# Performance work log

Hardware: AMD Instinct MI355X
Metric: run time of the kernel (lower is better)

The kernel has to match this reference:

```python
import jax, jax.numpy as jnp
from jax import lax
import numpy as np

B, DIM, HEADS, H, W = 4, 384, 8, 128, 128


def conv2d(x, w, b, groups=1, pad=0):
    # x: NCHW, w: OIHW (I = in_channels // groups)
    y = lax.conv_general_dilated(
        x, w, window_strides=(1, 1), padding=[(pad, pad), (pad, pad)],
        dimension_numbers=("NCHW", "OIHW", "NCHW"), feature_group_count=groups)
    return y + b[None, :, None, None]


def _l2norm(x, eps=1e-12):
    # torch F.normalize(dim=-1): x / max(||x||_2, eps)
    n = jnp.sqrt(jnp.sum(x * x, axis=-1, keepdims=True))
    return x / jnp.maximum(n, eps)


def setup_inputs() -> dict:
    key = jax.random.key(0)
    ks = jax.random.split(key, 8)
    s = 0.02
    d = DIM
    return {
        "x": jax.random.normal(ks[0], (B, d, H, W), jnp.float32),
        "feature": jax.random.normal(ks[1], (B, d, H, W), jnp.float32),
        "qkv_w": jax.random.normal(ks[2], (3 * d, d, 1, 1), jnp.float32) * s,
        "qkv_b": jnp.zeros((3 * d,), jnp.float32),
        "dw_w": jax.random.normal(ks[3], (3 * d, 1, 3, 3), jnp.float32) * s,  # depthwise, groups=3d
        "dw_b": jnp.zeros((3 * d,), jnp.float32),
        "qdw_w": jax.random.normal(ks[4], (2 * d, 1, 3, 3), jnp.float32) * s,  # depthwise, groups=2d
        "qdw_b": jnp.zeros((2 * d,), jnp.float32),
        "qpw_w": jax.random.normal(ks[5], (d, 2 * d, 1, 1), jnp.float32) * s,
        "qpw_b": jnp.zeros((d,), jnp.float32),
        "proj_w": jax.random.normal(ks[6], (d, d, 1, 1), jnp.float32) * s,
        "proj_b": jnp.zeros((d,), jnp.float32),
        "temperature": jnp.ones((HEADS, 1, 1), jnp.float32),
        "K": 24,  # top-k count == int(C * 0.5) with C = DIM // HEADS = 48
    }


def reference(x, feature, qkv_w, qkv_b, dw_w, dw_b, qdw_w, qdw_b,
              qpw_w, qpw_b, proj_w, proj_b, temperature, K):
    b, c, h, w = x.shape
    # qkv = dwconv3x3(conv1x1(x))
    qkv = conv2d(conv2d(x, qkv_w, qkv_b), dw_w, dw_b, groups=3 * c, pad=1)
    q, k, v = jnp.split(qkv, 3, axis=1)
    # q branch: dwconv3x3 on cat([q, feature]) -> GELU(exact) -> 1x1 conv
    qf = conv2d(jnp.concatenate([q, feature], axis=1), qdw_w, qdw_b, groups=2 * c, pad=1)
    qf = jax.nn.gelu(qf, approximate=False)
    q = conv2d(qf, qpw_w, qpw_b)

    def heads(t):
        return t.reshape(b, HEADS, c // HEADS, h * w)  # b head C (h w)

    q = _l2norm(heads(q))
    k = _l2norm(heads(k))
    v = heads(v)
    # channel attention: [b,head,C,C]
    attn = jnp.einsum("bhcn,bhdn->bhcd", q, k) * temperature
    vals, idx = lax.top_k(attn, K)
    neg = jnp.full_like(attn, -jnp.inf)
    attn = jnp.put_along_axis(neg, idx, vals, axis=-1, inplace=False)
    attn = jax.nn.softmax(attn, axis=-1)
    out = jnp.einsum("bhcd,bhdn->bhcn", attn, v).reshape(b, c, h, w)
    return conv2d(out, proj_w, proj_b)
```

## Files before the change

### kernel.cpp

```cpp
#include <hip/hip_runtime.h>

using u16 = unsigned short;
typedef __attribute__((ext_vector_type(8))) __bf16 bf16x8;
typedef __attribute__((ext_vector_type(4))) float  f32x4;
typedef __attribute__((ext_vector_type(8))) u16    u16x8;
typedef __attribute__((ext_vector_type(4))) u16    u16x4;

#define NB   4
#define DIM  384
#define NPIX 16384

__device__ __forceinline__ u16 f2bf(float f) {
  return __builtin_bit_cast(u16, (__bf16)f);
}
__device__ __forceinline__ float bf2f(u16 u) {
  return (float)__builtin_bit_cast(__bf16, u);
}
__device__ __forceinline__ void gload16(const void* g, void* l) {
  __builtin_amdgcn_global_load_lds(
      (const __attribute__((address_space(1))) void*)g,
      (__attribute__((address_space(3))) void*)l, 16, 0, 0);
}

__global__ void k_cvt2(const float* __restrict__ s, u16* __restrict__ hi,
                       u16* __restrict__ lo, int n) {
  int i = blockIdx.x * 256 + threadIdx.x;
  if (i < n) {
    float v = s[i];
    u16 h = f2bf(v);
    hi[i] = h;
    lo[i] = f2bf(v - bf2f(h));
  }
}

__global__ void k_splitx(const float* __restrict__ x, u16* __restrict__ xhi,
                         u16* __restrict__ xlo) {
  __shared__ float tile[32][33];
  int n0 = blockIdx.x * 32, c0 = blockIdx.y * 32, b = blockIdx.z;
  int tj = threadIdx.x & 31, ti = threadIdx.x >> 5;
  const float* xp = x + ((size_t)b * DIM + c0) * NPIX + n0;
  #pragma unroll
  for (int i = ti; i < 32; i += 8) tile[i][tj] = xp[(size_t)i * NPIX + tj];
  __syncthreads();
  const size_t ob = ((size_t)b * NPIX + n0) * DIM + c0;
  #pragma unroll
  for (int j = ti; j < 32; j += 8) {
    float v = tile[tj][j];
    u16 h = f2bf(v);
    xhi[ob + (size_t)j * DIM + tj] = h;
    xlo[ob + (size_t)j * DIM + tj] = f2bf(v - bf2f(h));
  }
}

template<int OUTMODE>
__global__ __launch_bounds__(256, 4)
void k_gemmS(const u16* __restrict__ A, const u16* __restrict__ B,
             void* __restrict__ Out, const float* __restrict__ bias,
             int M, int N, int Kd, size_t Astride)
{
  __shared__ u16 lA[128 * 64];
  __shared__ u16 lB[128 * 64];
  const int tid = threadIdx.x, wid = tid >> 6, lane = tid & 63;
  const int GX = gridDim.x, GY = gridDim.y;
  const int W = GX * GY * (int)gridDim.z;
  const int w = blockIdx.x + GX * (blockIdx.y + GY * blockIdx.z);
  const int nw = (w & 7) * (W >> 3) + (w >> 3);
  const int mt = nw % GY;
  const int rest = nw / GY;
  const int ntile = rest % GX;
  const int b = rest / GX;
  const int m0 = mt * 128, n0 = ntile * 128;

  const int srow = lane >> 3;
  const int sslot = (lane & 7) ^ srow;
  const size_t rowA = (size_t)(m0 + wid * 32 + srow) * Kd + sslot * 8 +
                      (size_t)b * Astride;
  const size_t rowB = ((size_t)b * N + n0 + wid * 32 + srow) * Kd + sslot * 8;
  u16* lAw = &lA[(wid * 32) * 64];
  u16* lBw = &lB[(wid * 32) * 64];
  const int wm = (wid & 1) * 64, wn = (wid >> 1) * 64;
  const int cl = lane & 15, rl = lane >> 4;
  const int sxa = cl & 7;

  f32x4 acc[4][4];
  const f32x4 fz = {0.f, 0.f, 0.f, 0.f};
  #pragma unroll
  for (int i = 0; i < 4; ++i)
    #pragma unroll
    for (int j = 0; j < 4; ++j) acc[i][j] = fz;

  const int nk = Kd >> 6;
  for (int kt = 0; kt < nk; ++kt) {
    const u16* Ap = A + rowA + kt * 64;
    const u16* Bp = B + rowB + kt * 64;
    __syncthreads();
    #pragma unroll
    for (int i = 0; i < 4; ++i) {
      gload16(Ap + (size_t)(i * 8) * Kd, lAw + i * 8 * 64);
      gload16(Bp + (size_t)(i * 8) * Kd, lBw + i * 8 * 64);
    }
    __syncthreads();
    #pragma unroll
    for (int ks = 0; ks < 2; ++ks) {
      bf16x8 av[4], bv[4];
      #pragma unroll
      for (int i = 0; i < 4; ++i) {
        av[i] = *(const bf16x8*)&lA[(wm + i * 16 + cl) * 64 + ((ks * 4 + rl) ^ sxa) * 8];
        bv[i] = *(const bf16x8*)&lB[(wn + i * 16 + cl) * 64 + ((ks * 4 + rl) ^ sxa) * 8];
      }
      #pragma unroll
      for (int i = 0; i < 4; ++i)
        #pragma unroll
        for (int j = 0; j < 4; ++j)
          acc[i][j] = __builtin_amdgcn_mfma_f32_16x16x32_bf16(av[i], bv[j], acc[i][j], 0, 0, 0);
    }
  }

  #pragma unroll
  for (int i = 0; i < 4; ++i) {
    #pragma unroll
    for (int j = 0; j < 4; ++j) {
      #pragma unroll
      for (int r = 0; r < 4; ++r) {
        const int m = m0 + wm + i * 16 + rl * 4 + r;
        const int n = n0 + wn + j * 16 + cl;
        const float v = acc[i][j][r] + bias[m];
        const size_t o = ((size_t)b * M + m) * N + n;
        if (OUTMODE == 0) ((float*)Out)[o] = v;
        else ((u16*)Out)[o] = f2bf(v);
      }
    }
  }
}

template<int OUTMODE, bool SSQ>
__global__ __launch_bounds__(256, 4)
void k_gemmP(const u16* __restrict__ Ahi, const u16* __restrict__ Alo,
             const u16* __restrict__ Bhi, const u16* __restrict__ Blo,
             void* __restrict__ Out, u16* __restrict__ OutLo,
             const float* __restrict__ bias, float* __restrict__ ssq,
             int M, int N, int Kd)
{
  __shared__ u16 lA[128 * 64];
  __shared__ u16 lB[128 * 64];
  const int tid = threadIdx.x, wid = tid >> 6, lane = tid & 63;
  const int GX = gridDim.x, GY = gridDim.y;
  const int W = GX * GY * (int)gridDim.z;
  const int w = blockIdx.x + GX * (blockIdx.y + GY * blockIdx.z);
  const int nw = (w & 7) * (W >> 3) + (w >> 3);
  const int mt = nw % GY;
  const int rest = nw / GY;
  const int ntile = rest % GX;
  const int b = rest / GX;
  const int m0 = mt * 128, n0 = ntile * 128;

  const int srow = lane >> 3;
  const int sp = (lane & 7) ^ srow;
  const int scol = (sp & 3) * 8;
  const u16* baseA = (sp < 4) ? Ahi : Alo;
  const u16* baseB = (sp < 4) ? Bhi : Blo;
  const u16* srcA[4];
  const u16* srcB[4];
  #pragma unroll
  for (int i = 0; i < 4; ++i) {
    srcA[i] = baseA + (size_t)(m0 + wid * 32 + i * 8 + srow) * Kd + scol;
    srcB[i] = baseB + ((size_t)b * N + n0 + wid * 32 + i * 8 + srow) * Kd + scol;
  }
  u16* lAw = &lA[(wid * 32) * 64];
  u16* lBw = &lB[(wid * 32) * 64];
  const int wm = (wid & 1) * 64, wn = (wid >> 1) * 64;
  const int cl = lane & 15, rl = lane >> 4;
  const int ph = rl ^ (cl & 7);

  f32x4 acc[4][4];
  const f32x4 fz = {0.f, 0.f, 0.f, 0.f};
  #pragma unroll
  for (int i = 0; i < 4; ++i)
    #pragma unroll
    for (int j = 0; j < 4; ++j) acc[i][j] = fz;

  const int nk = Kd >> 5;
  for (int kt = 0; kt < nk; ++kt) {
    __syncthreads();
    #pragma unroll
    for (int i = 0; i < 4; ++i) {
      gload16(srcA[i] + kt * 32, lAw + i * 8 * 64);
      gload16(srcB[i] + kt * 32, lBw + i * 8 * 64);
    }
    __syncthreads();
    bf16x8 avh[4], bvh[4], avl[4], bvl[4];
    #pragma unroll
    for (int i = 0; i < 4; ++i) {
      avh[i] = *(const bf16x8*)&lA[(wm + i * 16 + cl) * 64 + ph * 8];
      bvh[i] = *(const bf16x8*)&lB[(wn + i * 16 + cl) * 64 + ph * 8];
    }
    #pragma unroll
    for (int i = 0; i < 4; ++i)
      #pragma unroll
      for (int j = 0; j < 4; ++j)
        acc[i][j] = __builtin_amdgcn_mfma_f32_16x16x32_bf16(avh[i], bvh[j], acc[i][j], 0, 0, 0);
    #pragma unroll
    for (int i = 0; i < 4; ++i)
      avl[i] = *(const bf16x8*)&lA[(wm + i * 16 + cl) * 64 + (ph ^ 4) * 8];
    #pragma unroll
    for (int i = 0; i < 4; ++i)
      #pragma unroll
      for (int j = 0; j < 4; ++j)
        acc[i][j] = __builtin_amdgcn_mfma_f32_16x16x32_bf16(avl[i], bvh[j], acc[i][j], 0, 0, 0);
    #pragma unroll
    for (int i = 0; i < 4; ++i)
      bvl[i] = *(const bf16x8*)&lB[(wn + i * 16 + cl) * 64 + (ph ^ 4) * 8];
    #pragma unroll
    for (int i = 0; i < 4; ++i)
      #pragma unroll
      for (int j = 0; j < 4; ++j)
        acc[i][j] = __builtin_amdgcn_mfma_f32_16x16x32_bf16(avh[i], bvl[j], acc[i][j], 0, 0, 0);
  }

  float sq[4][4];
  if (SSQ) {
    #pragma unroll
    for (int i = 0; i < 4; ++i)
      #pragma unroll
      for (int r = 0; r < 4; ++r) sq[i][r] = 0.f;
  }
  #pragma unroll
  for (int i = 0; i < 4; ++i) {
    #pragma unroll
    for (int j = 0; j < 4; ++j) {
      #pragma unroll
      for (int r = 0; r < 4; ++r) {
        const int m = m0 + wm + i * 16 + rl * 4 + r;
        const int n = n0 + wn + j * 16 + cl;
        const float v = acc[i][j][r] + bias[m];
        if (SSQ) sq[i][r] += v * v;
        const size_t o = ((size_t)b * M + m) * N + n;
        if (OUTMODE == 0) ((float*)Out)[o] = v;
        else {
          u16 h = f2bf(v);
          ((u16*)Out)[o] = h;
          OutLo[o] = f2bf(v - bf2f(h));
        }
      }
    }
  }
  if (SSQ) {
    #pragma unroll
    for (int i = 0; i < 4; ++i) {
      #pragma unroll
      for (int r = 0; r < 4; ++r) {
        float s = sq[i][r];
        s += __shfl_xor(s, 1);
        s += __shfl_xor(s, 2);
        s += __shfl_xor(s, 4);
        s += __shfl_xor(s, 8);
        if (cl == 0)
          atomicAdd(&ssq[(size_t)b * M + m0 + wm + i * 16 + rl * 4 + r], s);
      }
    }
  }
}

__device__ __forceinline__ void row_acc_f32(const float* __restrict__ rowp,
    int x0, float w0, float w1, float w2,
    float& o0, float& o1, float& o2, float& o3)
{
  float4 r = *(const float4*)(rowp + x0);
  float lm = __shfl_up(r.w, 1);   if (x0 == 0)   lm = 0.f;
  float rt = __shfl_down(r.x, 1); if (x0 == 124) rt = 0.f;
  o0 = fmaf(lm,  w0, fmaf(r.x, w1, fmaf(r.y, w2, o0)));
  o1 = fmaf(r.x, w0, fmaf(r.y, w1, fmaf(r.z, w2, o1)));
  o2 = fmaf(r.y, w0, fmaf(r.z, w1, fmaf(r.w, w2, o2)));
  o3 = fmaf(r.z, w0, fmaf(r.w, w1, fmaf(rt,  w2, o3)));
}
__device__ __forceinline__ void row_acc_bf16(const u16* __restrict__ rowp,
    int x0, float w0, float w1, float w2,
    float& o0, float& o1, float& o2, float& o3)
{
  u16x4 rv = *(const u16x4*)(rowp + x0);
  float r0 = bf2f(rv[0]), r1 = bf2f(rv[1]), r2 = bf2f(rv[2]), r3 = bf2f(rv[3]);
  float lm = __shfl_up(r3, 1);   if (x0 == 0)   lm = 0.f;
  float rt = __shfl_down(r0, 1); if (x0 == 124) rt = 0.f;
  o0 = fmaf(lm, w0, fmaf(r0, w1, fmaf(r1, w2, o0)));
  o1 = fmaf(r0, w0, fmaf(r1, w1, fmaf(r2, w2, o1)));
  o2 = fmaf(r1, w0, fmaf(r2, w1, fmaf(r3, w2, o2)));
  o3 = fmaf(r2, w0, fmaf(r3, w1, fmaf(rt, w2, o3)));
}

__global__ __launch_bounds__(256, 4)
void k_dw3qk(const float* __restrict__ src, const float* __restrict__ w9,
             const float* __restrict__ bias, float* __restrict__ qdwbuf,
             u16* __restrict__ khi, u16* __restrict__ klo,
             float* __restrict__ ssqk)
{
  const int tid = threadIdx.x, wv = tid >> 6, lane = tid & 63;
  const int n0 = blockIdx.x * 1024 + tid * 4;
  const int h = n0 >> 7, x0 = n0 & 127;
  const int c0 = blockIdx.y * 8, b = blockIdx.z;
  const int hm = (h > 0) ? h - 1 : 0, hp = (h < 127) ? h + 1 : 127;
  const float topf = (h > 0) ? 1.f : 0.f, botf = (h < 127) ? 1.f : 0.f;
  const float* base = src + ((size_t)b * 768 + c0) * NPIX;
  const bool isk = (c0 >= 384);
  float ssl[8];
  #pragma unroll
  for (int s = 0; s < 8; ++s) {
    const int c = c0 + s;
    const float* sp = base + (size_t)s * NPIX;
    const float* wc = w9 + c * 9;
    const float bz = bias[c];
    float o0 = bz, o1 = bz, o2 = bz, o3 = bz;
    row_acc_f32(sp + hm * 128, x0, wc[0] * topf, wc[1] * topf, wc[2] * topf, o0, o1, o2, o3);
    row_acc_f32(sp + h  * 128, x0, wc[3], wc[4], wc[5], o0, o1, o2, o3);
    row_acc_f32(sp + hp * 128, x0, wc[6] * botf, wc[7] * botf, wc[8] * botf, o0, o1, o2, o3);
    if (!isk) {
      float4 ov = make_float4(o0, o1, o2, o3);
      *(float4*)(qdwbuf + ((size_t)b * 384 + c) * NPIX + n0) = ov;
      ssl[s] = 0.f;
    } else {
      ssl[s] = o0 * o0 + o1 * o1 + o2 * o2 + o3 * o3;
      u16x4 ph, pl;
      float oo[4] = {o0, o1, o2, o3};
      #pragma unroll
      for (int j = 0; j < 4; ++j) {
        u16 hv = f2bf(oo[j]);
        ph[j] = hv;
        pl[j] = f2bf(oo[j] - bf2f(hv));
      }
      const size_t off = ((size_t)b * 384 + (c - 384)) * NPIX + n0;
      *(u16x4*)(khi + off) = ph;
      *(u16x4*)(klo + off) = pl;
    }
  }
  if (isk) {
    __shared__ float sred[4][8];
    #pragma unroll
    for (int s = 0; s < 8; ++s) {
      float v = ssl[s];
      #pragma unroll
      for (int off = 32; off; off >>= 1) v += __shfl_down(v, off);
      if (lane == 0) sred[wv][s] = v;
    }
    __syncthreads();
    if (tid < 8) {
      float t = sred[0][tid] + sred[1][tid] + sred[2][tid] + sred[3][tid];
      atomicAdd(&ssqk[(size_t)b * DIM + (c0 - 384) + tid], t);
    }
  }
}

__global__ __launch_bounds__(512, 4)
void k_dw3vT(const u16* __restrict__ src, const float* __restrict__ w9,
             const float* __restrict__ bias, u16* __restrict__ vT)
{
  __shared__ u16 th[256 * 64];
  const int tid = threadIdx.x, wv = tid >> 6, lane = tid & 63;
  const int whw = blockIdx.x + 64 * (blockIdx.y + 6 * blockIdx.z);
  const int g = (whw & 7) + 8 * (whw >> 9);
  const int xchunk = (whw >> 3) & 63;
  const int cg = g % 6, b = g / 6;
  const int npx0 = xchunk * 256;
  const int n0 = npx0 + lane * 4;
  const int h = n0 >> 7, x0 = n0 & 127;
  const int c0 = cg * 64 + wv * 8;
  const int hm = (h > 0) ? h - 1 : 0, hp = (h < 127) ? h + 1 : 127;
  const float topf = (h > 0) ? 1.f : 0.f, botf = (h < 127) ? 1.f : 0.f;
  const u16* base = src + ((size_t)b * 384 + c0) * NPIX;
  u16x8 vh[4];
  #pragma unroll
  for (int s = 0; s < 8; ++s) {
    const int c = c0 + s;
    const u16* sp = base + (size_t)s * NPIX;
    const float* wc = w9 + c * 9;
    const float bz = bias[c];
    float o0 = bz, o1 = bz, o2 = bz, o3 = bz;
    row_acc_bf16(sp + hm * 128, x0, wc[0] * topf, wc[1] * topf, wc[2] * topf, o0, o1, o2, o3);
    row_acc_bf16(sp + h  * 128, x0, wc[3], wc[4], wc[5], o0, o1, o2, o3);
    row_acc_bf16(sp + hp * 128, x0, wc[6] * botf, wc[7] * botf, wc[8] * botf, o0, o1, o2, o3);
    vh[0][s] = f2bf(o0); vh[1][s] = f2bf(o1);
    vh[2][s] = f2bf(o2); vh[3][s] = f2bf(o3);
  }
  const int sl = (wv ^ (lane & 7)) * 8;
  #pragma unroll
  for (int j = 0; j < 4; ++j) {
    const int px = lane * 4 + j;
    *(u16x8*)&th[px * 64 + sl] = vh[j];
  }
  __syncthreads();
  if (tid < 256) {
    const int px = tid;
    u16* dst = vT + ((size_t)b * NPIX + npx0 + px) * 384 + cg * 64;
    const int rsw = (px >> 2) & 7;
    #pragma unroll
    for (int s = 0; s < 8; ++s)
      *(u16x8*)(dst + s * 8) = *(const u16x8*)&th[px * 64 + ((s ^ rsw) * 8)];
  }
}

__global__ __launch_bounds__(512, 4)
void k_qdw2(const float* __restrict__ qdwbuf, const float* __restrict__ feat,
            const float* __restrict__ w9, const float* __restrict__ bias,
            u16* __restrict__ qfhi, u16* __restrict__ qflo)
{
  __shared__ u16 th[256 * 64];
  __shared__ u16 tl[256 * 64];
  const int tid = threadIdx.x, wv = tid >> 6, lane = tid & 63;
  const int whw = blockIdx.x + 64 * (blockIdx.y + 12 * blockIdx.z);
  const int g = (whw & 7) + 8 * (whw >> 9);
  const int xchunk = (whw >> 3) & 63;
  const int cg = g % 12, b = g / 12;
  const int npx0 = xchunk * 256;
  const int n0 = npx0 + lane * 4;
  const int h = n0 >> 7, x0 = n0 & 127;
  const int c0 = cg * 64 + wv * 8;
  const int hm = (h > 0) ? h - 1 : 0, hp = (h < 127) ? h + 1 : 127;
  const float topf = (h > 0) ? 1.f : 0.f, botf = (h < 127) ? 1.f : 0.f;
  const bool isq = (c0 < 384);
  const float* base = isq ? (qdwbuf + ((size_t)b * 384 + c0) * NPIX)
                          : (feat   + ((size_t)b * 384 + (c0 - 384)) * NPIX);
  u16x8 vh[4], vl[4];
  #pragma unroll
  for (int s = 0; s < 8; ++s) {
    const int c = c0 + s;
    const float* sp = base + (size_t)s * NPIX;
    const float* wc = w9 + c * 9;
    const float bz = bias[c];
    float o0 = bz, o1 = bz, o2 = bz, o3 = bz;
    row_acc_f32(sp + hm * 128, x0, wc[0] * topf, wc[1] * topf, wc[2] * topf, o0, o1, o2, o3);
    row_acc_f32(sp + h  * 128, x0, wc[3], wc[4], wc[5], o0, o1, o2, o3);
    row_acc_f32(sp + hp * 128, x0, wc[6] * botf, wc[7] * botf, wc[8] * botf, o0, o1, o2, o3);
    float oo[4] = {o0, o1, o2, o3};
    #pragma unroll
    for (int j = 0; j < 4; ++j) {
      const float a = oo[j];
      const float g2 = 0.5f * a * (1.0f + erff(a * 0.70710678118654752440f));
      const u16 hv = f2bf(g2);
      vh[j][s] = hv;
      vl[j][s] = f2bf(g2 - bf2f(hv));
    }
  }
  const int sl = (wv ^ (lane & 7)) * 8;
  #pragma unroll
  for (int j = 0; j < 4; ++j) {
    const int px = lane * 4 + j;
    *(u16x8*)&th[px * 64 + sl] = vh[j];
    *(u16x8*)&tl[px * 64 + sl] = vl[j];
  }
  __syncthreads();
  const int sel = tid >> 8;
  const int px = tid & 255;
  const u16* srcb = sel ? tl : th;
  u16* dst = (sel ? qflo : qfhi) +
             ((size_t)b * NPIX + npx0 + px) * 768 + cg * 64;
  const int rsw = (px >> 2) & 7;
  #pragma unroll
  for (int s = 0; s < 8; ++s)
    *(u16x8*)(dst + s * 8) = *(const u16x8*)&srcb[px * 64 + ((s ^ rsw) * 8)];
}

__global__ __launch_bounds__(256)
void k_qk3(const u16* __restrict__ qhi, const u16* __restrict__ qlo,
           const u16* __restrict__ khi, const u16* __restrict__ klo,
           float* __restrict__ part)
{
  const int wid = threadIdx.x >> 6, lane = threadIdx.x & 63;
  const int bh = blockIdx.y;
  const int b = bh >> 3, hd = bh & 7;
  const size_t base = ((size_t)b * 384 + hd * 48) * NPIX;
  const int cl = lane & 15, rl = lane >> 4;
  f32x4 acc[3][3];
  const f32x4 fz = {0.f, 0.f, 0.f, 0.f};
  #pragma unroll
  for (int i = 0; i < 3; ++i)
    #pragma unroll
    for (int j = 0; j < 3; ++j) acc[i][j] = fz;
  for (int ck = 0; ck < 2; ++ck) {
    const int n0 = (blockIdx.x * 2 + ck) * 512 + wid * 128;
    #pragma unroll
    for (int ks = 0; ks < 4; ++ks) {
      const int nn = n0 + ks * 32 + rl * 8;
      bf16x8 ah[3], al[3], bh16[3], bl16[3];
      #pragma unroll
      for (int i = 0; i < 3; ++i) {
        const size_t ro = base + (size_t)(i * 16 + cl) * NPIX + nn;
        ah[i]   = *(const bf16x8*)&qhi[ro];
        al[i]   = *(const bf16x8*)&qlo[ro];
        bh16[i] = *(const bf16x8*)&khi[ro];
        bl16[i] = *(const bf16x8*)&klo[ro];
      }
      #pragma unroll
      for (int i = 0; i < 3; ++i)
        #pragma unroll
        for (int j = 0; j < 3; ++j) {
          acc[i][j] = __builtin_amdgcn_mfma_f32_16x16x32_bf16(ah[i], bh16[j], acc[i][j], 0, 0, 0);
          acc[i][j] = __builtin_amdgcn_mfma_f32_16x16x32_bf16(ah[i], bl16[j], acc[i][j], 0, 0, 0);
          acc[i][j] = __builtin_amdgcn_mfma_f32_16x16x32_bf16(al[i], bh16[j], acc[i][j], 0, 0, 0);
        }
    }
  }
  float* pp = part + ((size_t)bh * 64 + blockIdx.x * 4 + wid) * 2304;
  #pragma unroll
  for (int i = 0; i < 3; ++i)
    #pragma unroll
    for (int j = 0; j < 3; ++j)
      #pragma unroll
      for (int r = 0; r < 4; ++r)
        pp[(i * 16 + rl * 4 + r) * 48 + (j * 16 + cl)] = acc[i][j][r];
}

__global__ void k_qkred(const float* __restrict__ part, float* __restrict__ raw)
{
  const int bh = blockIdx.x;
  const int p = blockIdx.y * 256 + threadIdx.x;
  const float* pp = part + (size_t)bh * 64 * 2304 + p;
  float s = 0.f;
  #pragma unroll 8
  for (int w = 0; w < 64; ++w) s += pp[(size_t)w * 2304];
  raw[(size_t)bh * 2304 + p] = s;
}

__global__ void k_topk(const float* __restrict__ raw, const float* __restrict__ ssq_q,
                       const float* __restrict__ ssq_k, const float* __restrict__ temp,
                       const int* __restrict__ Kp, float* __restrict__ attn)
{
  const int bh = blockIdx.x, b = bh >> 3, hd = bh & 7;
  const int c = threadIdx.x;
  if (c >= 48) return;
  const int K = *Kp;
  const float qi = temp[hd] / fmaxf(sqrtf(ssq_q[b * DIM + hd * 48 + c]), 1e-12f);
  float vals[48];
  for (int d = 0; d < 48; ++d) {
    const float ki = 1.0f / fmaxf(sqrtf(ssq_k[b * DIM + hd * 48 + d]), 1e-12f);
    vals[d] = raw[(size_t)bh * 2304 + c * 48 + d] * qi * ki;
  }
  float mx = -3.0e38f;
  bool keep[48];
  for (int d = 0; d < 48; ++d) {
    int rank = 0;
    for (int e = 0; e < 48; ++e)
      rank += (vals[e] > vals[d] || (vals[e] == vals[d] && e < d)) ? 1 : 0;
    keep[d] = rank < K;
    if (keep[d]) mx = fmaxf(mx, vals[d]);
  }
  float sum = 0.f;
  for (int d = 0; d < 48; ++d) if (keep[d]) sum += expf(vals[d] - mx);
  const float rs = 1.0f / sum;
  float* ap = attn + (size_t)bh * 2304 + c * 48;
  for (int d = 0; d < 48; ++d) ap[d] = keep[d] ? expf(vals[d] - mx) * rs : 0.f;
}

__global__ void k_wa(const float* __restrict__ W, const float* __restrict__ attn,
                     u16* __restrict__ WaHi)
{
  const int bh = blockIdx.x, b = bh >> 3, hd = bh & 7;
  __shared__ float at[2304];
  for (int i = threadIdx.x; i < 2304; i += 256) at[i] = attn[(size_t)bh * 2304 + i];
  __syncthreads();
  for (int idx = threadIdx.x; idx < 384 * 48; idx += 256) {
    const int m = idx / 48, d = idx - m * 48;
    const float* wr = W + (size_t)m * 384 + hd * 48;
    float s = 0.f;
    #pragma unroll
    for (int c = 0; c < 48; ++c) s += wr[c] * at[c * 48 + d];
    WaHi[((size_t)b * 384 + m) * 384 + hd * 48 + d] = f2bf(s);
  }
}

extern "C" void kernel_launch(void* const* d_in, const int* in_sizes, int n_in,
                              void* d_out, int out_size, void* d_ws, size_t ws_size,
                              hipStream_t stream)
{
  (void)in_sizes; (void)n_in; (void)out_size; (void)ws_size;
  const float* x      = (const float*)d_in[0];
  const float* feat   = (const float*)d_in[1];
  const float* qkv_w  = (const float*)d_in[2];
  const float* qkv_b  = (const float*)d_in[3];
  const float* dw_w   = (const float*)d_in[4];
  const float* dw_b   = (const float*)d_in[5];
  const float* qdw_w  = (const float*)d_in[6];
  const float* qdw_b  = (const float*)d_in[7];
  const float* qpw_w  = (const float*)d_in[8];
  const float* qpw_b  = (const float*)d_in[9];
  const float* proj_w = (const float*)d_in[10];
  const float* proj_b = (const float*)d_in[11];
  const float* temp   = (const float*)d_in[12];
  const int*   Kp     = (const int*)d_in[13];

  char* ws = (char*)d_ws;
  const size_t HALF = 50331648;

  u16* WqkvHi = (u16*)ws;
  u16* WqkvLo = WqkvHi + 1152 * 384;
  u16* WqpwHi = WqkvLo + 1152 * 384;
  u16* WqpwLo = WqpwHi + 384 * 768;
  float* raw  = (float*)(ws + 3244032);
  float* attn = raw + (size_t)32 * 2304;
  float* ssqQ = attn + (size_t)32 * 2304;
  float* ssqK = ssqQ + NB * DIM;
  u16* WaHi   = (u16*)(ws + (4ull << 20));
  char* R1 = ws + (16ull << 20);
  u16* xThi = (u16*)R1;
  u16* xTlo = (u16*)(R1 + HALF);
  float* qdwbuf = (float*)R1;
  u16* qHi = (u16*)R1;
  u16* qLo = (u16*)(R1 + HALF);
  char* R2 = ws + (112ull << 20);
  float* qkpre = (float*)R2;
  u16* qfHi = (u16*)R2;
  u16* qfLo = (u16*)(R2 + 2 * HALF);
  float* part = (float*)R2;
  u16* vT   = (u16*)R2;
  u16* vpre = (u16*)(ws + (304ull << 20));
  u16* kHi = (u16*)d_out;
  u16* kLo = kHi + (size_t)NB * DIM * NPIX;

  hipMemsetAsync(ssqQ, 0, 2 * NB * DIM * sizeof(float), stream);
  k_cvt2<<<dim3(1728), 256, 0, stream>>>(qkv_w, WqkvHi, WqkvLo, 1152 * 384);
  k_cvt2<<<dim3(1152), 256, 0, stream>>>(qpw_w, WqpwHi, WqpwLo, 384 * 768);
  k_splitx<<<dim3(512, 12, NB), 256, 0, stream>>>(x, xThi, xTlo);
  k_gemmP<0, false><<<dim3(128, 6, NB), 256, 0, stream>>>(WqkvHi, WqkvLo, xThi, xTlo,
      (void*)qkpre, nullptr, qkv_b, nullptr, 768, NPIX, 384);
  k_gemmS<1><<<dim3(128, 3, NB), 256, 0, stream>>>(WqkvHi + (size_t)768 * 384,
      xThi, (void*)vpre, qkv_b + 768, 384, NPIX, 384, 0);
  k_dw3qk<<<dim3(16, 96, NB), 256, 0, stream>>>(qkpre, dw_w, dw_b, qdwbuf, kHi, kLo, ssqK);
  k_qdw2<<<dim3(64, 12, NB), 512, 0, stream>>>(qdwbuf, feat, qdw_w, qdw_b, qfHi, qfLo);
  k_gemmP<2, true><<<dim3(128, 3, NB), 256, 0, stream>>>(WqpwHi, WqpwLo, qfHi, qfLo,
      (void*)qHi, qLo, qpw_b, ssqQ, 384, NPIX, 768);
  k_qk3<<<dim3(16, 32), 256, 0, stream>>>(qHi, qLo, kHi, kLo, part);
  k_qkred<<<dim3(32, 9), 256, 0, stream>>>(part, raw);
  k_dw3vT<<<dim3(64, 6, NB), 512, 0, stream>>>(vpre, dw_w + 768 * 9, dw_b + 768, vT);
  k_topk<<<dim3(32), 64, 0, stream>>>(raw, ssqQ, ssqK, temp, Kp, attn);
  k_wa<<<dim3(32), 256, 0, stream>>>(proj_w, attn, WaHi);
  k_gemmS<0><<<dim3(128, 3, NB), 256, 0, stream>>>(WaHi, vT,
      d_out, proj_b, 384, NPIX, 384, (size_t)384 * 384);
}
```

Before: 896.4 us.

## Fuse attention reduction/topk/WA kernels, vectorize splitx stores, swizzle dw3qk blocks

Merges the partial-sum reduction, top-k softmax, and projection-weight mixing into one per-head kernel that keeps intermediates in shared memory. This removes two launches and the global round trips for raw and attn. It also widens the transpose tile in splitx to 64 channels, so each thread writes 8 bf16 values as one 16-byte store. It remaps dw3qk block indices to group neighbouring channel groups. The fused kernel runs the reduction on only 32 blocks, so the part read is much less parallel than the 288-block reduction it replaces.

```diff
diff --git a/kernel.cpp b/kernel.cpp
--- a/kernel.cpp
+++ b/kernel.cpp
@@ -35,21 +35,29 @@
 
 __global__ void k_splitx(const float* __restrict__ x, u16* __restrict__ xhi,
                          u16* __restrict__ xlo) {
-  __shared__ float tile[32][33];
-  int n0 = blockIdx.x * 32, c0 = blockIdx.y * 32, b = blockIdx.z;
-  int tj = threadIdx.x & 31, ti = threadIdx.x >> 5;
+  __shared__ float tile[64][33];
+  const int tid = threadIdx.x;
+  const int n0 = blockIdx.x * 32, c0 = blockIdx.y * 64, b = blockIdx.z;
+  const int tj = tid & 31, ti = tid >> 5;
   const float* xp = x + ((size_t)b * DIM + c0) * NPIX + n0;
   #pragma unroll
-  for (int i = ti; i < 32; i += 8) tile[i][tj] = xp[(size_t)i * NPIX + tj];
+  for (int i = 0; i < 8; ++i) {
+    const int c = i * 8 + ti;
+    tile[c][tj] = xp[(size_t)c * NPIX + tj];
+  }
   __syncthreads();
-  const size_t ob = ((size_t)b * NPIX + n0) * DIM + c0;
-  #pragma unroll
-  for (int j = ti; j < 32; j += 8) {
-    float v = tile[tj][j];
-    u16 h = f2bf(v);
-    xhi[ob + (size_t)j * DIM + tj] = h;
-    xlo[ob + (size_t)j * DIM + tj] = f2bf(v - bf2f(h));
-  }
+  const int px = tid >> 3, sl = tid & 7;
+  u16x8 ph, pl;
+  #pragma unroll
+  for (int e = 0; e < 8; ++e) {
+    const float v = tile[sl * 8 + e][px];
+    const u16 h = f2bf(v);
+    ph[e] = h;
+    pl[e] = f2bf(v - bf2f(h));
+  }
+  const size_t off = ((size_t)b * NPIX + n0 + px) * DIM + c0 + sl * 8;
+  *(u16x8*)(xhi + off) = ph;
+  *(u16x8*)(xlo + off) = pl;
 }
 
 template<int OUTMODE>
@@ -294,9 +302,13 @@
              float* __restrict__ ssqk)
 {
   const int tid = threadIdx.x, wv = tid >> 6, lane = tid & 63;
-  const int n0 = blockIdx.x * 1024 + tid * 4;
+  const int whw = blockIdx.x + 16 * (blockIdx.y + 96 * blockIdx.z);
+  const int g = (whw & 7) + 8 * (whw >> 7);
+  const int xchunk = (whw >> 3) & 15;
+  const int cg = g % 96, b = g / 96;
+  const int n0 = xchunk * 1024 + tid * 4;
   const int h = n0 >> 7, x0 = n0 & 127;
-  const int c0 = blockIdx.y * 8, b = blockIdx.z;
+  const int c0 = cg * 8;
   const int hm = (h > 0) ? h - 1 : 0, hp = (h < 127) ? h + 1 : 127;
   const float topf = (h > 0) ? 1.f : 0.f, botf = (h < 127) ? 1.f : 0.f;
   const float* base = src + ((size_t)b * 768 + c0) * NPIX;
@@ -507,55 +519,51 @@
         pp[(i * 16 + rl * 4 + r) * 48 + (j * 16 + cl)] = acc[i][j][r];
 }
 
-__global__ void k_qkred(const float* __restrict__ part, float* __restrict__ raw)
-{
-  const int bh = blockIdx.x;
-  const int p = blockIdx.y * 256 + threadIdx.x;
-  const float* pp = part + (size_t)bh * 64 * 2304 + p;
-  float s = 0.f;
-  #pragma unroll 8
-  for (int w = 0; w < 64; ++w) s += pp[(size_t)w * 2304];
-  raw[(size_t)bh * 2304 + p] = s;
-}
-
-__global__ void k_topk(const float* __restrict__ raw, const float* __restrict__ ssq_q,
+__global__ void k_attn(const float* __restrict__ part, const float* __restrict__ ssq_q,
                        const float* __restrict__ ssq_k, const float* __restrict__ temp,
-                       const int* __restrict__ Kp, float* __restrict__ attn)
-{
+                       const int* __restrict__ Kp, const float* __restrict__ W,
+                       u16* __restrict__ WaHi)
+{
+  __shared__ float rawL[2304];
+  __shared__ float at[2304];
   const int bh = blockIdx.x, b = bh >> 3, hd = bh & 7;
-  const int c = threadIdx.x;
-  if (c >= 48) return;
-  const int K = *Kp;
-  const float qi = temp[hd] / fmaxf(sqrtf(ssq_q[b * DIM + hd * 48 + c]), 1e-12f);
-  float vals[48];
-  for (int d = 0; d < 48; ++d) {
-    const float ki = 1.0f / fmaxf(sqrtf(ssq_k[b * DIM + hd * 48 + d]), 1e-12f);
-    vals[d] = raw[(size_t)bh * 2304 + c * 48 + d] * qi * ki;
-  }
-  float mx = -3.0e38f;
-  bool keep[48];
-  for (int d = 0; d < 48; ++d) {
-    int rank = 0;
-    for (int e = 0; e < 48; ++e)
-      rank += (vals[e] > vals[d] || (vals[e] == vals[d] && e < d)) ? 1 : 0;
-    keep[d] = rank < K;
-    if (keep[d]) mx = fmaxf(mx, vals[d]);
-  }
-  float sum = 0.f;
-  for (int d = 0; d < 48; ++d) if (keep[d]) sum += expf(vals[d] - mx);
-  const float rs = 1.0f / sum;
-  float* ap = attn + (size_t)bh * 2304 + c * 48;
-  for (int d = 0; d < 48; ++d) ap[d] = keep[d] ? expf(vals[d] - mx) * rs : 0.f;
-}
-
-__global__ void k_wa(const float* __restrict__ W, const float* __restrict__ attn,
-                     u16* __restrict__ WaHi)
-{
-  const int bh = blockIdx.x, b = bh >> 3, hd = bh & 7;
-  __shared__ float at[2304];
-  for (int i = threadIdx.x; i < 2304; i += 256) at[i] = attn[(size_t)bh * 2304 + i];
+  const int tid = threadIdx.x;
+  const float* pp = part + (size_t)bh * 64 * 2304;
+  #pragma unroll
+  for (int j = 0; j < 9; ++j) {
+    const int p = tid + j * 256;
+    float s = 0.f;
+    #pragma unroll 8
+    for (int w = 0; w < 64; ++w) s += pp[(size_t)w * 2304 + p];
+    rawL[p] = s;
+  }
   __syncthreads();
-  for (int idx = threadIdx.x; idx < 384 * 48; idx += 256) {
+  if (tid < 48) {
+    const int c = tid;
+    const int K = *Kp;
+    const float qi = temp[hd] / fmaxf(sqrtf(ssq_q[b * DIM + hd * 48 + c]), 1e-12f);
+    float vals[48];
+    for (int d = 0; d < 48; ++d) {
+      const float ki = 1.0f / fmaxf(sqrtf(ssq_k[b * DIM + hd * 48 + d]), 1e-12f);
+      vals[d] = rawL[c * 48 + d] * qi * ki;
+    }
+    float mx = -3.0e38f;
+    bool keep[48];
+    for (int d = 0; d < 48; ++d) {
+      int rank = 0;
+      for (int e = 0; e < 48; ++e)
+        rank += (vals[e] > vals[d] || (vals[e] == vals[d] && e < d)) ? 1 : 0;
+      keep[d] = rank < K;
+      if (keep[d]) mx = fmaxf(mx, vals[d]);
+    }
+    float sum = 0.f;
+    for (int d = 0; d < 48; ++d) if (keep[d]) sum += expf(vals[d] - mx);
+    const float rs = 1.0f / sum;
+    for (int d = 0; d < 48; ++d)
+      at[c * 48 + d] = keep[d] ? expf(vals[d] - mx) * rs : 0.f;
+  }
+  __syncthreads();
+  for (int idx = tid; idx < 384 * 48; idx += 256) {
     const int m = idx / 48, d = idx - m * 48;
     const float* wr = W + (size_t)m * 384 + hd * 48;
     float s = 0.f;
@@ -592,9 +600,7 @@
   u16* WqkvLo = WqkvHi + 1152 * 384;
   u16* WqpwHi = WqkvLo + 1152 * 384;
   u16* WqpwLo = WqpwHi + 384 * 768;
-  float* raw  = (float*)(ws + 3244032);
-  float* attn = raw + (size_t)32 * 2304;
-  float* ssqQ = attn + (size_t)32 * 2304;
+  float* ssqQ = (float*)(ws + 3244032);
   float* ssqK = ssqQ + NB * DIM;
   u16* WaHi   = (u16*)(ws + (4ull << 20));
   char* R1 = ws + (16ull << 20);
@@ -616,7 +622,7 @@
   hipMemsetAsync(ssqQ, 0, 2 * NB * DIM * sizeof(float), stream);
   k_cvt2<<<dim3(1728), 256, 0, stream>>>(qkv_w, WqkvHi, WqkvLo, 1152 * 384);
   k_cvt2<<<dim3(1152), 256, 0, stream>>>(qpw_w, WqpwHi, WqpwLo, 384 * 768);
-  k_splitx<<<dim3(512, 12, NB), 256, 0, stream>>>(x, xThi, xTlo);
+  k_splitx<<<dim3(512, 6, NB), 256, 0, stream>>>(x, xThi, xTlo);
   k_gemmP<0, false><<<dim3(128, 6, NB), 256, 0, stream>>>(WqkvHi, WqkvLo, xThi, xTlo,
       (void*)qkpre, nullptr, qkv_b, nullptr, 768, NPIX, 384);
   k_gemmS<1><<<dim3(128, 3, NB), 256, 0, stream>>>(WqkvHi + (size_t)768 * 384,
@@ -626,10 +632,8 @@
   k_gemmP<2, true><<<dim3(128, 3, NB), 256, 0, stream>>>(WqpwHi, WqpwLo, qfHi, qfLo,
       (void*)qHi, qLo, qpw_b, ssqQ, 384, NPIX, 768);
   k_qk3<<<dim3(16, 32), 256, 0, stream>>>(qHi, qLo, kHi, kLo, part);
-  k_qkred<<<dim3(32, 9), 256, 0, stream>>>(part, raw);
+  k_attn<<<dim3(32), 256, 0, stream>>>(part, ssqQ, ssqK, temp, Kp, proj_w, WaHi);
   k_dw3vT<<<dim3(64, 6, NB), 512, 0, stream>>>(vpre, dw_w + 768 * 9, dw_b + 768, vT);
-  k_topk<<<dim3(32), 64, 0, stream>>>(raw, ssqQ, ssqK, temp, Kp, attn);
-  k_wa<<<dim3(32), 256, 0, stream>>>(proj_w, attn, WaHi);
   k_gemmS<0><<<dim3(128, 3, NB), 256, 0, stream>>>(WaHi, vT,
       d_out, proj_b, 384, NPIX, 384, (size_t)384 * 384);
 }
```

Measured after the change: 895.5 us. Within noise of the previous version (-0.1%).
